# Kernel tuning notes

Measured on AMD Instinct MI355X. Metric: run time of the kernel, lower is better.

## Reference

```python
import jax, jax.numpy as jnp
import numpy as np

VEC_DIM = 128
N_DOCS = 100000
N_WORDS = 100000
B = 16384
CTX = 8
NS = 16


def setup_inputs() -> dict:
    key = jax.random.key(0)
    k1, k2, k3, k4, k5 = jax.random.split(key, 5)
    doc_ids = jax.random.randint(k1, (B,), 0, N_DOCS)
    context_ids = jax.random.randint(k2, (B, CTX), 0, N_WORDS)
    sample_ids = jax.random.randint(k3, (B, NS), 0, N_WORDS)
    paragraph_matrix = jax.random.normal(k4, (N_DOCS, VEC_DIM), dtype=jnp.float32)
    word_matrix = jax.random.normal(k5, (N_WORDS, VEC_DIM), dtype=jnp.float32)
    outputs = jnp.zeros((VEC_DIM, N_WORDS), dtype=jnp.float32)
    return {
        "doc_ids": doc_ids,
        "context_ids": context_ids,
        "sample_ids": sample_ids,
        "paragraph_matrix": paragraph_matrix,
        "word_matrix": word_matrix,
        "outputs": outputs,
    }


def reference(doc_ids, context_ids, sample_ids, paragraph_matrix, word_matrix, outputs):
    # inputs: [B, D] = doc embedding + sum of context word embeddings
    inputs = paragraph_matrix[doc_ids] + jnp.sum(word_matrix[context_ids], axis=1)
    # sampled output columns: [B, D, NS]
    out_cols = outputs[:, sample_ids].transpose(1, 0, 2)
    # batched dot products: [B, NS]
    return jnp.einsum("bd,bds->bs", inputs, out_cols)
```

## Files before the change

kernel.cpp:

```cpp
#include <hip/hip_runtime.h>

#define VEC_D   128
#define N_WORDS 100000
#define BATCH   16384
#define CTX     8
#define NS      16

typedef float f32x4 __attribute__((ext_vector_type(4)));

__global__ __launch_bounds__(256) void transpose_kernel(
    const float* __restrict__ src,
    float* __restrict__ dst)
{
    __shared__ float lds[32][VEC_D + 1];
    const int tid = threadIdx.x;
    const int w0  = blockIdx.x * 32;

    #pragma unroll
    for (int p = 0; p < 4; ++p) {
        const int d = p * 32 + (tid >> 3);
        const int w = (tid & 7) * 4;
        const f32x4 v = __builtin_nontemporal_load(
            (const f32x4*)&src[(size_t)d * N_WORDS + w0 + w]);
        lds[w + 0][d] = v.x;
        lds[w + 1][d] = v.y;
        lds[w + 2][d] = v.z;
        lds[w + 3][d] = v.w;
    }
    __syncthreads();

    #pragma unroll
    for (int p = 0; p < 4; ++p) {
        const int wl = p * 8 + (tid >> 5);
        const int d4 = (tid & 31) * 4;
        f32x4 v;
        v.x = lds[wl][d4 + 0];
        v.y = lds[wl][d4 + 1];
        v.z = lds[wl][d4 + 2];
        v.w = lds[wl][d4 + 3];
        *(f32x4*)&dst[(size_t)(w0 + wl) * VEC_D + d4] = v;
    }
}

template <bool TRANSPOSED>
__global__ __launch_bounds__(256) void dm_kernel(
    const int*   __restrict__ doc_ids,
    const int*   __restrict__ context_ids,
    const int*   __restrict__ sample_ids,
    const float* __restrict__ pm,
    const float* __restrict__ wm,
    const float* __restrict__ outsrc,
    float*       __restrict__ out)
{
    const int tid = threadIdx.x;
    const int l   = tid & 15;
    const int b   = blockIdx.x * 16 + (tid >> 4);
    const int d0  = l * 8;

    const int doc = doc_ids[b];
    const f32x4* pr = (const f32x4*)&pm[(size_t)doc * VEC_D + d0];
    f32x4 v0 = pr[0], v1 = pr[1];
    #pragma unroll
    for (int c = 0; c < CTX; ++c) {
        const int wid = context_ids[b * CTX + c];
        const f32x4* wr = (const f32x4*)&wm[(size_t)wid * VEC_D + d0];
        v0 += wr[0];
        v1 += wr[1];
    }

    float acc[NS];
    #pragma unroll
    for (int s = 0; s < NS; ++s) {
        const int wid = sample_ids[b * NS + s];
        if (TRANSPOSED) {
            const f32x4* orow = (const f32x4*)&outsrc[(size_t)wid * VEC_D + d0];
            const f32x4 o0 = orow[0], o1 = orow[1];
            acc[s] = v0.x * o0.x + v0.y * o0.y + v0.z * o0.z + v0.w * o0.w
                   + v1.x * o1.x + v1.y * o1.y + v1.z * o1.z + v1.w * o1.w;
        } else {
            float a = 0.0f;
            #pragma unroll
            for (int k = 0; k < 4; ++k)
                a += v0[k] * outsrc[(size_t)(d0 + k) * N_WORDS + wid];
            #pragma unroll
            for (int k = 0; k < 4; ++k)
                a += v1[k] * outsrc[(size_t)(d0 + 4 + k) * N_WORDS + wid];
            acc[s] = a;
        }
    }

    #pragma unroll
    for (int j = 0; j < 4; ++j) {
        const int m = 1 << j;
        const int h = 8 >> j;
        const bool hi = (l & m) != 0;
        #pragma unroll
        for (int i = 0; i < h; ++i) {
            const float send = hi ? acc[i] : acc[h + i];
            const float recv = __shfl_xor(send, m, 64);
            acc[i] = (hi ? acc[h + i] : acc[i]) + recv;
        }
    }
    const int s = ((l & 1) << 3) | ((l & 2) << 1) | ((l & 4) >> 1) | ((l & 8) >> 3);
    out[(size_t)b * NS + s] = acc[0];
}

extern "C" void kernel_launch(void* const* d_in, const int* in_sizes, int n_in,
                              void* d_out, int out_size, void* d_ws, size_t ws_size,
                              hipStream_t stream) {
    const int*   doc_ids     = (const int*)d_in[0];
    const int*   context_ids = (const int*)d_in[1];
    const int*   sample_ids  = (const int*)d_in[2];
    const float* pm          = (const float*)d_in[3];
    const float* wm          = (const float*)d_in[4];
    const float* outputs     = (const float*)d_in[5];
    float*       out         = (float*)d_out;

    const size_t transposed_bytes = (size_t)N_WORDS * VEC_D * sizeof(float);

    if (ws_size >= transposed_bytes) {
        float* outT = (float*)d_ws;
        transpose_kernel<<<N_WORDS / 32, 256, 0, stream>>>(outputs, outT);
        dm_kernel<true><<<BATCH / 16, 256, 0, stream>>>(
            doc_ids, context_ids, sample_ids, pm, wm, outT, out);
    } else {
        dm_kernel<false><<<BATCH / 16, 256, 0, stream>>>(
            doc_ids, context_ids, sample_ids, pm, wm, outputs, out);
    }
}
```

Measured before the change: 53.78 us.

## Use 32 lanes per batch row with vectorized index loads in dm_kernel

Each batch row is now handled by 32 lanes holding 4 floats each instead of 16 lanes holding 8, which doubles the thread count and the grid size. Context and sample ids are read as int4 vectors, and the row gathers are issued in groups of four so more loads are in flight. An extra shuffle step combines the two half-rows, after which only half the lanes write output. Launch bounds now request 8 blocks per CU. This trades more shuffles and idle store lanes for more parallelism and memory-level concurrency on the random gathers.

```diff
diff --git a/kernel.cpp b/kernel.cpp
--- a/kernel.cpp
+++ b/kernel.cpp
@@ -7,6 +7,7 @@
 #define NS      16
 
 typedef float f32x4 __attribute__((ext_vector_type(4)));
+typedef int   i32x4 __attribute__((ext_vector_type(4)));
 
 __global__ __launch_bounds__(256) void transpose_kernel(
     const float* __restrict__ src,
@@ -43,7 +44,7 @@
 }
 
 template <bool TRANSPOSED>
-__global__ __launch_bounds__(256) void dm_kernel(
+__global__ __launch_bounds__(256, 8) void dm_kernel(
     const int*   __restrict__ doc_ids,
     const int*   __restrict__ context_ids,
     const int*   __restrict__ sample_ids,
@@ -53,47 +54,58 @@
     float*       __restrict__ out)
 {
     const int tid = threadIdx.x;
-    const int l   = tid & 15;
-    const int b   = blockIdx.x * 16 + (tid >> 4);
-    const int d0  = l * 8;
+    const int r   = tid & 31;
+    const int b   = blockIdx.x * 8 + (tid >> 5);
+    const int d0  = r * 4;
 
     const int doc = doc_ids[b];
-    const f32x4* pr = (const f32x4*)&pm[(size_t)doc * VEC_D + d0];
-    f32x4 v0 = pr[0], v1 = pr[1];
+    f32x4 v = *(const f32x4*)&pm[(size_t)doc * VEC_D + d0];
+
+    const i32x4* cid = (const i32x4*)&context_ids[b * CTX];
     #pragma unroll
-    for (int c = 0; c < CTX; ++c) {
-        const int wid = context_ids[b * CTX + c];
-        const f32x4* wr = (const f32x4*)&wm[(size_t)wid * VEC_D + d0];
-        v0 += wr[0];
-        v1 += wr[1];
+    for (int g = 0; g < 2; ++g) {
+        const i32x4 c4 = cid[g];
+        f32x4 w[4];
+        #pragma unroll
+        for (int k = 0; k < 4; ++k)
+            w[k] = *(const f32x4*)&wm[(size_t)c4[k] * VEC_D + d0];
+        #pragma unroll
+        for (int k = 0; k < 4; ++k)
+            v += w[k];
     }
 
     float acc[NS];
+    const i32x4* sid = (const i32x4*)&sample_ids[b * NS];
     #pragma unroll
-    for (int s = 0; s < NS; ++s) {
-        const int wid = sample_ids[b * NS + s];
+    for (int g = 0; g < 4; ++g) {
+        const i32x4 s4 = sid[g];
         if (TRANSPOSED) {
-            const f32x4* orow = (const f32x4*)&outsrc[(size_t)wid * VEC_D + d0];
-            const f32x4 o0 = orow[0], o1 = orow[1];
-            acc[s] = v0.x * o0.x + v0.y * o0.y + v0.z * o0.z + v0.w * o0.w
-                   + v1.x * o1.x + v1.y * o1.y + v1.z * o1.z + v1.w * o1.w;
-        } else {
-            float a = 0.0f;
+            f32x4 o[4];
             #pragma unroll
             for (int k = 0; k < 4; ++k)
-                a += v0[k] * outsrc[(size_t)(d0 + k) * N_WORDS + wid];
+                o[k] = *(const f32x4*)&outsrc[(size_t)s4[k] * VEC_D + d0];
             #pragma unroll
             for (int k = 0; k < 4; ++k)
-                a += v1[k] * outsrc[(size_t)(d0 + 4 + k) * N_WORDS + wid];
-            acc[s] = a;
+                acc[g * 4 + k] = v.x * o[k].x + v.y * o[k].y
+                               + v.z * o[k].z + v.w * o[k].w;
+        } else {
+            #pragma unroll
+            for (int k = 0; k < 4; ++k) {
+                float a = 0.0f;
+                #pragma unroll
+                for (int q = 0; q < 4; ++q)
+                    a += v[q] * outsrc[(size_t)(d0 + q) * N_WORDS + s4[k]];
+                acc[g * 4 + k] = a;
+            }
         }
     }
 
+    const int l4 = r & 15;
     #pragma unroll
     for (int j = 0; j < 4; ++j) {
         const int m = 1 << j;
         const int h = 8 >> j;
-        const bool hi = (l & m) != 0;
+        const bool hi = (l4 & m) != 0;
         #pragma unroll
         for (int i = 0; i < h; ++i) {
             const float send = hi ? acc[i] : acc[h + i];
@@ -101,8 +113,12 @@
             acc[i] = (hi ? acc[h + i] : acc[i]) + recv;
         }
     }
-    const int s = ((l & 1) << 3) | ((l & 2) << 1) | ((l & 4) >> 1) | ((l & 8) >> 3);
-    out[(size_t)b * NS + s] = acc[0];
+    acc[0] += __shfl_xor(acc[0], 16, 64);
+
+    if (r < 16) {
+        const int s = ((r & 1) << 3) | ((r & 2) << 1) | ((r & 4) >> 1) | ((r & 8) >> 3);
+        out[(size_t)b * NS + s] = acc[0];
+    }
 }
 
 extern "C" void kernel_launch(void* const* d_in, const int* in_sizes, int n_in,
@@ -121,10 +137,10 @@
     if (ws_size >= transposed_bytes) {
         float* outT = (float*)d_ws;
         transpose_kernel<<<N_WORDS / 32, 256, 0, stream>>>(outputs, outT);
-        dm_kernel<true><<<BATCH / 16, 256, 0, stream>>>(
+        dm_kernel<true><<<BATCH / 8, 256, 0, stream>>>(
             doc_ids, context_ids, sample_ids, pm, wm, outT, out);
     } else {
-        dm_kernel<false><<<BATCH / 16, 256, 0, stream>>>(
+        dm_kernel<false><<<BATCH / 8, 256, 0, stream>>>(
             doc_ids, context_ids, sample_ids, pm, wm, outputs, out);
     }
 }
```

Result: slower. 58.53 us (+8.8%).
